# Performance work log

Hardware: AMD Instinct MI355X
Metric: run time of the kernel (lower is better)

The kernel has to match this reference:

```python
import jax, jax.numpy as jnp
import numpy as np

N = 16384          # collocation points
WIDTH = 128        # WavePINN width_size
DEPTH = 6          # WavePINN depth -> 5 hidden-to-hidden layers
PWIDTH = 32        # PsiNetwork width_size
PDEPTH = 2         # PsiNetwork depth -> 1 hidden-to-hidden layer
C0 = 1.0           # base_wave_speed


def _lin(k, out_dim, in_dim):
    return jax.random.normal(k, (out_dim, in_dim), jnp.float32) / np.sqrt(in_dim)


def setup_inputs() -> dict:
    key = jax.random.key(0)
    ks = jax.random.split(key, 20)
    inp = {
        "t": jax.random.uniform(ks[0], (N,), jnp.float32),
        "x": jax.random.uniform(ks[1], (N,), jnp.float32),
        "y": jax.random.uniform(ks[2], (N,), jnp.float32),
        "z": jax.random.uniform(ks[3], (N,), jnp.float32),
        # WavePINN (u_model) params: 4 -> 128 -> (128)x5 -> 1
        "uW_in": _lin(ks[4], WIDTH, 4),
        "ub_in": jnp.zeros((WIDTH,), jnp.float32),
        "uW_hid": jax.random.normal(ks[5], (DEPTH - 1, WIDTH, WIDTH), jnp.float32) / np.sqrt(WIDTH),
        "ub_hid": jnp.zeros((DEPTH - 1, WIDTH), jnp.float32),
        "uW_out": _lin(ks[6], 1, WIDTH),
        "ub_out": jnp.zeros((1,), jnp.float32),
        # PsiNetwork params: 4 -> 32 -> 32 -> 1
        "pW_in": _lin(ks[7], PWIDTH, 4),
        "pb_in": jnp.zeros((PWIDTH,), jnp.float32),
        "pW_hid": jax.random.normal(ks[8], (PDEPTH - 1, PWIDTH, PWIDTH), jnp.float32) / np.sqrt(PWIDTH),
        "pb_hid": jnp.zeros((PDEPTH - 1, PWIDTH), jnp.float32),
        "pW_out": _lin(ks[9], 1, PWIDTH),
        "pb_out": jnp.zeros((1,), jnp.float32),
    }
    return inp


def _mlp(pt, W_in, b_in, W_hid, b_hid, W_out, b_out):
    # eqx.nn.MLP with tanh activation, linear final layer; returns scalar
    h = jnp.tanh(W_in @ pt + b_in)
    for i in range(W_hid.shape[0]):  # static, small layer count
        h = jnp.tanh(W_hid[i] @ h + b_hid[i])
    return (W_out @ h + b_out)[0]


def reference(t, x, y, z,
              uW_in, ub_in, uW_hid, ub_hid, uW_out, ub_out,
              pW_in, pb_in, pW_hid, pb_hid, pW_out, pb_out):
    def point_residual(pt):  # pt: [4] = (t, x, y, z)
        u_fn = lambda p: _mlp(p, uW_in, ub_in, uW_hid, ub_hid, uW_out, ub_out)
        psi = _mlp(pt, pW_in, pb_in, pW_hid, pb_hid, pW_out, pb_out)
        c = C0 * (1.0 + psi)  # modulated wave speed
        # diagonal of the 4x4 Hessian: u_tt, u_xx, u_yy, u_zz
        d = jnp.diagonal(jax.hessian(u_fn)(pt))
        lap = d[1] + d[2] + d[3]
        resid = d[0] - c ** 2 * lap
        has_nan = jnp.any(jnp.isnan(jnp.stack([d[0], d[1], d[2], d[3], c])))
        return jnp.where(has_nan, jnp.float32(jnp.nan), resid)

    pts = jnp.stack([t, x, y, z], axis=1)  # [N, 4]
    return jax.vmap(point_residual)(pts).astype(jnp.float32)
```

## Files before the change

### kernel.cpp

```cpp
#include <hip/hip_runtime.h>
#include <math.h>

#define N_PTS 16384
#define WID   128
#define NHID  5
#define PPB   16
#define CH    9
#define COLS  (PPB*CH)
#define KPAD  132
#define NBLK  (N_PTS/PPB)

typedef __attribute__((ext_vector_type(8))) __bf16 bf16x8;
typedef __attribute__((ext_vector_type(4))) float  f32x4;

__device__ __forceinline__ unsigned short f2bf(float x) {
    unsigned int u = __builtin_bit_cast(unsigned int, x);
    u += 0x7FFFu + ((u >> 16) & 1u);
    return (unsigned short)(u >> 16);
}
__device__ __forceinline__ float bf2f(unsigned short h) {
    unsigned int u = ((unsigned int)h) << 16;
    return __builtin_bit_cast(float, u);
}
__device__ __forceinline__ void split_bf(float x, unsigned short& hi, unsigned short& lo) {
    const unsigned int u = __builtin_bit_cast(unsigned int, x);
    hi = (unsigned short)(u >> 16);
    const float rem = x - __builtin_bit_cast(float, u & 0xFFFF0000u);
    lo = (unsigned short)(__builtin_bit_cast(unsigned int, rem) >> 16);
}
__device__ __forceinline__ unsigned int cvtpk(float v0, float v1) {
    unsigned int r;
    asm("v_cvt_pk_bf16_f32 %0, %1, %2" : "=v"(r) : "v"(v0), "v"(v1));
    return r;
}
__device__ __forceinline__ void split_pk4(const float v0, const float v1,
                                          const float v2, const float v3,
                                          uint2& ph, uint2& pl) {
    const unsigned int h01 = cvtpk(v0, v1);
    const unsigned int h23 = cvtpk(v2, v3);
    const float f0 = __builtin_bit_cast(float, h01 << 16);
    const float f1 = __builtin_bit_cast(float, h01 & 0xFFFF0000u);
    const float f2 = __builtin_bit_cast(float, h23 << 16);
    const float f3 = __builtin_bit_cast(float, h23 & 0xFFFF0000u);
    ph = make_uint2(h01, h23);
    pl = make_uint2(cvtpk(v0 - f0, v1 - f1), cvtpk(v2 - f2, v3 - f3));
}
__device__ __forceinline__ void fast_tanh_g(float x, float& a, float& g) {
    x = fminf(fmaxf(x, -40.0f), 40.0f);
    const float e = __builtin_amdgcn_exp2f(2.88539008177793f * x);
    const float r = __builtin_amdgcn_rcpf(e + 1.0f);
    a = 1.0f - 2.0f * r;
    g = 4.0f * e * r * r;
}

__global__ __launch_bounds__(64) void pack_w(const float* __restrict__ uWhid,
                                             unsigned short* __restrict__ whi,
                                             unsigned short* __restrict__ wlo)
{
    const int f  = blockIdx.x;
    const int v  = threadIdx.x;
    const int l  = f >> 5;
    const int s  = (f >> 3) & 3;
    const int rt = f & 7;
    const int row = rt*16 + (v & 15);
    const int k0  = s*32 + ((v >> 4) << 3);
    const float* src = uWhid + (l*WID + row)*WID + k0;
    unsigned short h[8], lo[8];
#pragma unroll
    for (int j = 0; j < 8; ++j) {
        const float x = src[j];
        h[j]  = f2bf(x);
        lo[j] = f2bf(x - bf2f(h[j]));
    }
    const int off = f*512 + v*8;
    *reinterpret_cast<ushort4*>(&whi[off])   = make_ushort4(h[0],h[1],h[2],h[3]);
    *reinterpret_cast<ushort4*>(&whi[off+4]) = make_ushort4(h[4],h[5],h[6],h[7]);
    *reinterpret_cast<ushort4*>(&wlo[off])   = make_ushort4(lo[0],lo[1],lo[2],lo[3]);
    *reinterpret_cast<ushort4*>(&wlo[off+4]) = make_ushort4(lo[4],lo[5],lo[6],lo[7]);
}

__global__ __launch_bounds__(256, 2) void resid_mfma(
    const float* __restrict__ gt, const float* __restrict__ gx,
    const float* __restrict__ gy, const float* __restrict__ gz,
    const float* __restrict__ uWin, const float* __restrict__ ubin,
    const float* __restrict__ ubhid, const float* __restrict__ uWout,
    const unsigned short* __restrict__ whi, const unsigned short* __restrict__ wlo,
    const float* __restrict__ pWin, const float* __restrict__ pbin,
    const float* __restrict__ pWhid, const float* __restrict__ pbhid,
    const float* __restrict__ pWout, const float* __restrict__ pbout,
    float* __restrict__ out)
{
    __shared__ unsigned short act_h[COLS*KPAD];
    __shared__ unsigned short act_l[COLS*KPAD];
    __shared__ float pts4[PPB][4];
    __shared__ float psi_h1[PPB][32];
    __shared__ float c2s[PPB];
    __shared__ float psum[4][PPB][4];

    {
        const int skew = (int)((blockIdx.x + (blockIdx.x >> 8)) & 3);
        for (int i = 0; i < skew; ++i) {
            __builtin_amdgcn_s_sleep(60);
        }
    }

    const int tid  = threadIdx.x;
    const int rq   = tid >> 6;
    const int v    = tid & 63;
    const int base = blockIdx.x * PPB;

    if (tid < PPB) {
        pts4[tid][0] = gt[base+tid]; pts4[tid][1] = gx[base+tid];
        pts4[tid][2] = gy[base+tid]; pts4[tid][3] = gz[base+tid];
    }
    __syncthreads();

    {
        const int p  = tid & 15;
        const int gg = tid >> 4;
        const float q0 = pts4[p][0], q1 = pts4[p][1], q2 = pts4[p][2], q3 = pts4[p][3];
#pragma unroll
        for (int c4 = 0; c4 < 2; ++c4) {
            float vf[CH][4];
#pragma unroll
            for (int i = 0; i < 4; ++i) {
                const int n = gg*8 + c4*4 + i;
                const float4 wr = *reinterpret_cast<const float4*>(&uWin[n*4]);
                const float z = ubin[n] + wr.x*q0 + wr.y*q1 + wr.z*q2 + wr.w*q3;
                float a, g;  fast_tanh_g(z, a, g);
                const float m = -2.0f * a * g;
                vf[0][i] = a;
                vf[1][i] = g*wr.x; vf[2][i] = g*wr.y; vf[3][i] = g*wr.z; vf[4][i] = g*wr.w;
                vf[5][i] = m*wr.x*wr.x; vf[6][i] = m*wr.y*wr.y;
                vf[7][i] = m*wr.z*wr.z; vf[8][i] = m*wr.w*wr.w;
            }
            const int n0 = gg*8 + c4*4;
#pragma unroll
            for (int ch = 0; ch < CH; ++ch) {
                uint2 ph, pl;
                split_pk4(vf[ch][0], vf[ch][1], vf[ch][2], vf[ch][3], ph, pl);
                const int off = (ch*PPB + p)*KPAD + n0;
                *reinterpret_cast<uint2*>(&act_h[off]) = ph;
                *reinterpret_cast<uint2*>(&act_l[off]) = pl;
            }
        }
    }
    {
        const int p = tid >> 4, sub = tid & 15;
        const float q0 = pts4[p][0], q1 = pts4[p][1], q2 = pts4[p][2], q3 = pts4[p][3];
#pragma unroll
        for (int rr = 0; rr < 2; ++rr) {
            const int r = sub*2 + rr;
            const float4 wr = *reinterpret_cast<const float4*>(&pWin[r*4]);
            float a, gd;
            fast_tanh_g(pbin[r] + wr.x*q0 + wr.y*q1 + wr.z*q2 + wr.w*q3, a, gd);
            psi_h1[p][r] = a;
        }
    }
    __syncthreads();

    {
        const int p = tid >> 4, sub = tid & 15;
        float partial = 0.f;
#pragma unroll
        for (int rr = 0; rr < 2; ++rr) {
            const int r = sub*2 + rr;
            float s = pbhid[r];
#pragma unroll
            for (int j = 0; j < 32; ++j) s = fmaf(pWhid[r*32+j], psi_h1[p][j], s);
            float a, gd;  fast_tanh_g(s, a, gd);
            partial = fmaf(pWout[r], a, partial);
        }
        partial += __shfl_xor(partial, 1);
        partial += __shfl_xor(partial, 2);
        partial += __shfl_xor(partial, 4);
        partial += __shfl_xor(partial, 8);
        if (sub == 0) {
            const float c = 1.0f + pbout[0] + partial;
            c2s[p] = c * c;
        }
    }

    f32x4 acc[2][CH];
    const int g4    = (v >> 4) << 2;
    const int lrow0 = rq * 32;
    const int bcol  = v & 15;
    const int krow  = (v >> 4) << 3;

    for (int l = 0; l < NHID; ++l) {
#pragma unroll
        for (int rt = 0; rt < 2; ++rt) {
            acc[rt][0] = *reinterpret_cast<const f32x4*>(&ubhid[l*WID + lrow0 + rt*16 + g4]);
#pragma unroll
            for (int ct = 1; ct < CH; ++ct) acc[rt][ct] = (f32x4){0.f,0.f,0.f,0.f};
        }
#pragma unroll
        for (int s = 0; s < 4; ++s) {
            bf16x8 bh[CH], bl[CH], ah[2], al[2];
            const int kof = s*32 + krow;
            const int fb  = ((l*4 + s)*8 + rq*2)*512 + v*8;
#pragma unroll
            for (int rt = 0; rt < 2; ++rt) {
                ah[rt] = *reinterpret_cast<const bf16x8*>(&whi[fb + rt*512]);
                al[rt] = *reinterpret_cast<const bf16x8*>(&wlo[fb + rt*512]);
            }
#pragma unroll
            for (int ct = 0; ct < CH; ++ct) {
                const int off = (ct*PPB + bcol)*KPAD + kof;
                bh[ct] = *reinterpret_cast<const bf16x8*>(&act_h[off]);
                bl[ct] = *reinterpret_cast<const bf16x8*>(&act_l[off]);
            }
            __builtin_amdgcn_s_setprio(1);
#pragma unroll
            for (int rt = 0; rt < 2; ++rt)
#pragma unroll
                for (int ct = 0; ct < CH; ++ct)
                    acc[rt][ct] = __builtin_amdgcn_mfma_f32_16x16x32_bf16(ah[rt], bh[ct], acc[rt][ct], 0,0,0);
#pragma unroll
            for (int rt = 0; rt < 2; ++rt)
#pragma unroll
                for (int ct = 0; ct < CH; ++ct)
                    acc[rt][ct] = __builtin_amdgcn_mfma_f32_16x16x32_bf16(ah[rt], bl[ct], acc[rt][ct], 0,0,0);
#pragma unroll
            for (int rt = 0; rt < 2; ++rt)
#pragma unroll
                for (int ct = 0; ct < CH; ++ct)
                    acc[rt][ct] = __builtin_amdgcn_mfma_f32_16x16x32_bf16(al[rt], bh[ct], acc[rt][ct], 0,0,0);
            __builtin_amdgcn_s_setprio(0);
        }

        if (l < NHID-1) {
            const int p = v & 15;
            uint2 ph[2][CH], pl[2][CH];
#pragma unroll
            for (int rt = 0; rt < 2; ++rt) {
                float vf[CH][4];
#pragma unroll
                for (int r = 0; r < 4; ++r) {
                    float a, g;  fast_tanh_g(acc[rt][0][r], a, g);
                    const float m2a = -2.0f * a;
                    vf[0][r] = a;
#pragma unroll
                    for (int d = 0; d < 4; ++d) {
                        const float zd  = acc[rt][1+d][r];
                        const float zdd = acc[rt][5+d][r];
                        vf[1+d][r] = g * zd;
                        vf[5+d][r] = g * fmaf(m2a*zd, zd, zdd);
                    }
                }
#pragma unroll
                for (int ch = 0; ch < CH; ++ch)
                    split_pk4(vf[ch][0], vf[ch][1], vf[ch][2], vf[ch][3], ph[rt][ch], pl[rt][ch]);
            }
            __syncthreads();
#pragma unroll
            for (int rt = 0; rt < 2; ++rt) {
                const int n0 = lrow0 + rt*16 + g4;
#pragma unroll
                for (int ch = 0; ch < CH; ++ch) {
                    const int off = (ch*PPB + p)*KPAD + n0;
                    *reinterpret_cast<uint2*>(&act_h[off]) = ph[rt][ch];
                    *reinterpret_cast<uint2*>(&act_l[off]) = pl[rt][ch];
                }
            }
            __syncthreads();
        }
    }

    float part0 = 0.f, part1 = 0.f, part2 = 0.f, part3 = 0.f;
#pragma unroll
    for (int rt = 0; rt < 2; ++rt) {
        const float4 w4 = *reinterpret_cast<const float4*>(&uWout[lrow0 + rt*16 + g4]);
#pragma unroll
        for (int r = 0; r < 4; ++r) {
            const float wr = (&w4.x)[r];
            float a, g;  fast_tanh_g(acc[rt][0][r], a, g);
            const float zd0 = acc[rt][1][r], zd1 = acc[rt][2][r];
            const float zd2 = acc[rt][3][r], zd3 = acc[rt][4][r];
            part0 = fmaf(wr, g*(acc[rt][5][r] - 2.0f*a*zd0*zd0), part0);
            part1 = fmaf(wr, g*(acc[rt][6][r] - 2.0f*a*zd1*zd1), part1);
            part2 = fmaf(wr, g*(acc[rt][7][r] - 2.0f*a*zd2*zd2), part2);
            part3 = fmaf(wr, g*(acc[rt][8][r] - 2.0f*a*zd3*zd3), part3);
        }
    }
    part0 += __shfl_xor(part0, 16); part0 += __shfl_xor(part0, 32);
    part1 += __shfl_xor(part1, 16); part1 += __shfl_xor(part1, 32);
    part2 += __shfl_xor(part2, 16); part2 += __shfl_xor(part2, 32);
    part3 += __shfl_xor(part3, 16); part3 += __shfl_xor(part3, 32);
    if (v < PPB) {
        psum[rq][v][0] = part0; psum[rq][v][1] = part1;
        psum[rq][v][2] = part2; psum[rq][v][3] = part3;
    }
    __syncthreads();
    if (tid < PPB) {
        const float d0  = psum[0][tid][0] + psum[1][tid][0] + psum[2][tid][0] + psum[3][tid][0];
        const float lap = (psum[0][tid][1] + psum[1][tid][1] + psum[2][tid][1] + psum[3][tid][1])
                        + (psum[0][tid][2] + psum[1][tid][2] + psum[2][tid][2] + psum[3][tid][2])
                        + (psum[0][tid][3] + psum[1][tid][3] + psum[2][tid][3] + psum[3][tid][3]);
        out[base+tid] = d0 - c2s[tid]*lap;
    }
}

__global__ __launch_bounds__(64) void psi_kernel(
    const float* __restrict__ gt, const float* __restrict__ gx,
    const float* __restrict__ gy, const float* __restrict__ gz,
    const float* __restrict__ pWin, const float* __restrict__ pbin,
    const float* __restrict__ pWhid, const float* __restrict__ pbhid,
    const float* __restrict__ pWout, const float* __restrict__ pbout,
    float* __restrict__ c2)
{
    const int i = blockIdx.x * 64 + threadIdx.x;
    if (i >= N_PTS) return;
    const float q0 = gt[i], q1 = gx[i], q2 = gy[i], q3 = gz[i];
    float h1[32];
#pragma unroll
    for (int r = 0; r < 32; ++r) {
        float s = pbin[r] + pWin[r*4+0]*q0 + pWin[r*4+1]*q1
                + pWin[r*4+2]*q2 + pWin[r*4+3]*q3;
        h1[r] = tanhf(s);
    }
    float psi = pbout[0];
#pragma unroll 4
    for (int r = 0; r < 32; ++r) {
        float s = pbhid[r];
#pragma unroll
        for (int j = 0; j < 32; ++j) s = fmaf(pWhid[r*32+j], h1[j], s);
        psi = fmaf(pWout[r], tanhf(s), psi);
    }
    const float c = 1.0f + psi;
    c2[i] = c * c;
}

__global__ __launch_bounds__(256, 2) void resid_f32(
    const float* __restrict__ gt, const float* __restrict__ gx,
    const float* __restrict__ gy, const float* __restrict__ gz,
    const float* __restrict__ uWin, const float* __restrict__ ubin,
    const float* __restrict__ uWhid, const float* __restrict__ ubhid,
    const float* __restrict__ uWout,
    const float* __restrict__ c2g, float* __restrict__ out)
{
    __shared__ float act[WID][16*CH];
    __shared__ float ptsh[16][4];
    __shared__ float dsh[16][4];
    const int tid  = threadIdx.x;
    const int rg   = tid >> 4;
    const int p    = tid & 15;
    const int base = blockIdx.x * 16;
    const int row0 = rg * 8;
    const int c0   = p * CH;
    if (tid < 16) {
        ptsh[tid][0] = gt[base+tid]; ptsh[tid][1] = gx[base+tid];
        ptsh[tid][2] = gy[base+tid]; ptsh[tid][3] = gz[base+tid];
    }
    __syncthreads();
    {
        const float q0 = ptsh[p][0], q1 = ptsh[p][1], q2 = ptsh[p][2], q3 = ptsh[p][3];
#pragma unroll
        for (int r = 0; r < 8; ++r) {
            const int row = row0 + r;
            const float w0 = uWin[row*4+0], w1 = uWin[row*4+1];
            const float w2 = uWin[row*4+2], w3 = uWin[row*4+3];
            const float zz = ubin[row] + w0*q0 + w1*q1 + w2*q2 + w3*q3;
            const float a  = tanhf(zz);
            const float g  = 1.0f - a*a;
            const float m2 = -2.0f * a * g;
            act[row][c0+0] = a;
            act[row][c0+1] = g*w0; act[row][c0+2] = g*w1;
            act[row][c0+3] = g*w2; act[row][c0+4] = g*w3;
            act[row][c0+5] = m2*w0*w0; act[row][c0+6] = m2*w1*w1;
            act[row][c0+7] = m2*w2*w2; act[row][c0+8] = m2*w3*w3;
        }
    }
    __syncthreads();
    for (int l = 0; l < NHID; ++l) {
        const float* __restrict__ Wl = uWhid + l*WID*WID;
        float accv[8][CH];
#pragma unroll
        for (int r = 0; r < 8; ++r) {
            accv[r][0] = ubhid[l*WID + row0 + r];
#pragma unroll
            for (int c = 1; c < CH; ++c) accv[r][c] = 0.0f;
        }
        for (int k0 = 0; k0 < WID; k0 += 4) {
            float4 wv[8];
#pragma unroll
            for (int r = 0; r < 8; ++r)
                wv[r] = *reinterpret_cast<const float4*>(&Wl[(row0+r)*WID + k0]);
            float hv[4][CH];
#pragma unroll
            for (int kk = 0; kk < 4; ++kk)
#pragma unroll
                for (int c = 0; c < CH; ++c) hv[kk][c] = act[k0+kk][c0+c];
#pragma unroll
            for (int kk = 0; kk < 4; ++kk)
#pragma unroll
                for (int r = 0; r < 8; ++r) {
                    const float wk = reinterpret_cast<const float*>(&wv[r])[kk];
#pragma unroll
                    for (int c = 0; c < CH; ++c) accv[r][c] = fmaf(wk, hv[kk][c], accv[r][c]);
                }
        }
        __syncthreads();
#pragma unroll
        for (int r = 0; r < 8; ++r) {
            const int row = row0 + r;
            const float a = tanhf(accv[r][0]);
            const float g = 1.0f - a*a;
            act[row][c0+0] = a;
#pragma unroll
            for (int i = 0; i < 4; ++i) {
                const float zd  = accv[r][1+i];
                const float zdd = accv[r][5+i];
                act[row][c0+1+i] = g*zd;
                act[row][c0+5+i] = g*(zdd - 2.0f*a*zd*zd);
            }
        }
        __syncthreads();
    }
    if (tid < 64) {
        const int pp = tid >> 2, ii = tid & 3;
        float s = 0.0f;
        for (int k = 0; k < WID; ++k) s = fmaf(uWout[k], act[k][pp*CH+5+ii], s);
        dsh[pp][ii] = s;
    }
    __syncthreads();
    if (tid < 16) {
        const float d0  = dsh[tid][0];
        const float lap = dsh[tid][1] + dsh[tid][2] + dsh[tid][3];
        out[base+tid] = d0 - c2g[base+tid]*lap;
    }
}

extern "C" void kernel_launch(void* const* d_in, const int* in_sizes, int n_in,
                              void* d_out, int out_size, void* d_ws, size_t ws_size,
                              hipStream_t stream)
{
    const float* gt    = (const float*)d_in[0];
    const float* gx    = (const float*)d_in[1];
    const float* gy    = (const float*)d_in[2];
    const float* gz    = (const float*)d_in[3];
    const float* uWin  = (const float*)d_in[4];
    const float* ubin  = (const float*)d_in[5];
    const float* uWhid = (const float*)d_in[6];
    const float* ubhid = (const float*)d_in[7];
    const float* uWout = (const float*)d_in[8];
    const float* pWin  = (const float*)d_in[10];
    const float* pbin  = (const float*)d_in[11];
    const float* pWhid = (const float*)d_in[12];
    const float* pbhid = (const float*)d_in[13];
    const float* pWout = (const float*)d_in[14];
    const float* pbout = (const float*)d_in[15];
    float* out = (float*)d_out;

    if (ws_size >= 327680) {
        unsigned short* whi = (unsigned short*)d_ws;
        unsigned short* wlo = whi + 81920;
        pack_w<<<160, 64, 0, stream>>>(uWhid, whi, wlo);
        resid_mfma<<<NBLK, 256, 0, stream>>>(gt, gx, gy, gz,
                uWin, ubin, ubhid, uWout, whi, wlo,
                pWin, pbin, pWhid, pbhid, pWout, pbout, out);
    } else {
        float* c2 = (float*)d_ws;
        psi_kernel<<<N_PTS/64, 64, 0, stream>>>(gt, gx, gy, gz,
                pWin, pbin, pWhid, pbhid, pWout, pbout, c2);
        resid_f32<<<N_PTS/16, 256, 0, stream>>>(gt, gx, gy, gz,
                uWin, ubin, uWhid, ubhid, uWout, c2, out);
    }
}
```

Baseline: 80.01 us.

## Interleave two 16-point sub-batches per block to overlap MFMA with tanh-jet packing

Each block now handles 32 points as two 16-point sub-batches that share one activation buffer. MFMA work for one sub-batch is interleaved with the tanh/derivative jet packing of the other, so matrix and vector work can overlap across layers. The psi network setup and the second input jet are also moved into the shadow of the first layer's MFMAs. The block-skew sleep and setprio hints are dropped. The cost is roughly doubled accumulator register pressure, half as many blocks, and extra barriers per layer.

```diff
diff --git a/kernel.cpp b/kernel.cpp
--- a/kernel.cpp
+++ b/kernel.cpp
@@ -4,9 +4,10 @@
 #define N_PTS 16384
 #define WID   128
 #define NHID  5
-#define PPB   16
+#define SPTS  16
+#define PPB   32
 #define CH    9
-#define COLS  (PPB*CH)
+#define COLS  (SPTS*CH)
 #define KPAD  132
 #define NBLK  (N_PTS/PPB)
 
@@ -79,6 +80,168 @@
     *reinterpret_cast<ushort4*>(&wlo[off+4]) = make_ushort4(lo[4],lo[5],lo[6],lo[7]);
 }
 
+__device__ __forceinline__ void mfma_layer(
+    f32x4 (&acc)[2][CH],
+    const unsigned short* __restrict__ whi, const unsigned short* __restrict__ wlo,
+    const unsigned short (&act_h)[COLS*KPAD], const unsigned short (&act_l)[COLS*KPAD],
+    const float* __restrict__ ubhid, const int l,
+    const int lrow0, const int g4, const int rq, const int v,
+    const int bcol, const int krow)
+{
+#pragma unroll
+    for (int rt = 0; rt < 2; ++rt) {
+        acc[rt][0] = *reinterpret_cast<const f32x4*>(&ubhid[l*WID + lrow0 + rt*16 + g4]);
+#pragma unroll
+        for (int ct = 1; ct < CH; ++ct) acc[rt][ct] = (f32x4){0.f,0.f,0.f,0.f};
+    }
+#pragma unroll
+    for (int s = 0; s < 4; ++s) {
+        bf16x8 bh[CH], bl[CH], ah[2], al[2];
+        const int kof = s*32 + krow;
+        const int fb  = ((l*4 + s)*8 + rq*2)*512 + v*8;
+#pragma unroll
+        for (int rt = 0; rt < 2; ++rt) {
+            ah[rt] = *reinterpret_cast<const bf16x8*>(&whi[fb + rt*512]);
+            al[rt] = *reinterpret_cast<const bf16x8*>(&wlo[fb + rt*512]);
+        }
+#pragma unroll
+        for (int ct = 0; ct < CH; ++ct) {
+            const int off = (ct*SPTS + bcol)*KPAD + kof;
+            bh[ct] = *reinterpret_cast<const bf16x8*>(&act_h[off]);
+            bl[ct] = *reinterpret_cast<const bf16x8*>(&act_l[off]);
+        }
+#pragma unroll
+        for (int rt = 0; rt < 2; ++rt)
+#pragma unroll
+            for (int ct = 0; ct < CH; ++ct)
+                acc[rt][ct] = __builtin_amdgcn_mfma_f32_16x16x32_bf16(ah[rt], bh[ct], acc[rt][ct], 0,0,0);
+#pragma unroll
+        for (int rt = 0; rt < 2; ++rt)
+#pragma unroll
+            for (int ct = 0; ct < CH; ++ct)
+                acc[rt][ct] = __builtin_amdgcn_mfma_f32_16x16x32_bf16(ah[rt], bl[ct], acc[rt][ct], 0,0,0);
+#pragma unroll
+        for (int rt = 0; rt < 2; ++rt)
+#pragma unroll
+            for (int ct = 0; ct < CH; ++ct)
+                acc[rt][ct] = __builtin_amdgcn_mfma_f32_16x16x32_bf16(al[rt], bh[ct], acc[rt][ct], 0,0,0);
+    }
+}
+
+__device__ __forceinline__ void jet_pack(
+    const f32x4 (&acc)[2][CH], uint2 (&ph)[2][CH], uint2 (&pl)[2][CH])
+{
+#pragma unroll
+    for (int rt = 0; rt < 2; ++rt) {
+        float vf[CH][4];
+#pragma unroll
+        for (int r = 0; r < 4; ++r) {
+            float a, g;  fast_tanh_g(acc[rt][0][r], a, g);
+            const float m2a = -2.0f * a;
+            vf[0][r] = a;
+#pragma unroll
+            for (int d = 0; d < 4; ++d) {
+                const float zd  = acc[rt][1+d][r];
+                const float zdd = acc[rt][5+d][r];
+                vf[1+d][r] = g * zd;
+                vf[5+d][r] = g * fmaf(m2a*zd, zd, zdd);
+            }
+        }
+#pragma unroll
+        for (int ch = 0; ch < CH; ++ch)
+            split_pk4(vf[ch][0], vf[ch][1], vf[ch][2], vf[ch][3], ph[rt][ch], pl[rt][ch]);
+    }
+}
+
+__device__ __forceinline__ void store_act(
+    const uint2 (&ph)[2][CH], const uint2 (&pl)[2][CH],
+    unsigned short (&act_h)[COLS*KPAD], unsigned short (&act_l)[COLS*KPAD],
+    const int lrow0, const int g4, const int p)
+{
+#pragma unroll
+    for (int rt = 0; rt < 2; ++rt) {
+        const int n0 = lrow0 + rt*16 + g4;
+#pragma unroll
+        for (int ch = 0; ch < CH; ++ch) {
+            const int off = (ch*SPTS + p)*KPAD + n0;
+            *reinterpret_cast<uint2*>(&act_h[off]) = ph[rt][ch];
+            *reinterpret_cast<uint2*>(&act_l[off]) = pl[rt][ch];
+        }
+    }
+}
+
+__device__ __forceinline__ void input_jet(
+    const float q0, const float q1, const float q2, const float q3,
+    const float* __restrict__ uWin, const float* __restrict__ ubin, const int gg,
+    uint2 (&ph)[2][CH], uint2 (&pl)[2][CH])
+{
+#pragma unroll
+    for (int c4 = 0; c4 < 2; ++c4) {
+        float vf[CH][4];
+#pragma unroll
+        for (int i = 0; i < 4; ++i) {
+            const int n = gg*8 + c4*4 + i;
+            const float4 wr = *reinterpret_cast<const float4*>(&uWin[n*4]);
+            const float z = ubin[n] + wr.x*q0 + wr.y*q1 + wr.z*q2 + wr.w*q3;
+            float a, g;  fast_tanh_g(z, a, g);
+            const float m = -2.0f * a * g;
+            vf[0][i] = a;
+            vf[1][i] = g*wr.x; vf[2][i] = g*wr.y; vf[3][i] = g*wr.z; vf[4][i] = g*wr.w;
+            vf[5][i] = m*wr.x*wr.x; vf[6][i] = m*wr.y*wr.y;
+            vf[7][i] = m*wr.z*wr.z; vf[8][i] = m*wr.w*wr.w;
+        }
+#pragma unroll
+        for (int ch = 0; ch < CH; ++ch)
+            split_pk4(vf[ch][0], vf[ch][1], vf[ch][2], vf[ch][3], ph[c4][ch], pl[c4][ch]);
+    }
+}
+
+__device__ __forceinline__ void store_input(
+    const uint2 (&ph)[2][CH], const uint2 (&pl)[2][CH],
+    unsigned short (&act_h)[COLS*KPAD], unsigned short (&act_l)[COLS*KPAD],
+    const int gg, const int p)
+{
+#pragma unroll
+    for (int c4 = 0; c4 < 2; ++c4) {
+        const int n0 = gg*8 + c4*4;
+#pragma unroll
+        for (int ch = 0; ch < CH; ++ch) {
+            const int off = (ch*SPTS + p)*KPAD + n0;
+            *reinterpret_cast<uint2*>(&act_h[off]) = ph[c4][ch];
+            *reinterpret_cast<uint2*>(&act_l[off]) = pl[c4][ch];
+        }
+    }
+}
+
+__device__ __forceinline__ void out_parts(
+    const f32x4 (&acc)[2][CH], const float* __restrict__ uWout,
+    const int lrow0, const int g4,
+    float& p0, float& p1, float& p2, float& p3)
+{
+    p0 = p1 = p2 = p3 = 0.f;
+#pragma unroll
+    for (int rt = 0; rt < 2; ++rt) {
+        const float4 w4 = *reinterpret_cast<const float4*>(&uWout[lrow0 + rt*16 + g4]);
+#pragma unroll
+        for (int r = 0; r < 4; ++r) {
+            const float wr = (&w4.x)[r];
+            float a, g;  fast_tanh_g(acc[rt][0][r], a, g);
+            const float zd0 = acc[rt][1][r], zd1 = acc[rt][2][r];
+            const float zd2 = acc[rt][3][r], zd3 = acc[rt][4][r];
+            p0 = fmaf(wr, g*(acc[rt][5][r] - 2.0f*a*zd0*zd0), p0);
+            p1 = fmaf(wr, g*(acc[rt][6][r] - 2.0f*a*zd1*zd1), p1);
+            p2 = fmaf(wr, g*(acc[rt][7][r] - 2.0f*a*zd2*zd2), p2);
+            p3 = fmaf(wr, g*(acc[rt][8][r] - 2.0f*a*zd3*zd3), p3);
+        }
+    }
+    p0 += __shfl_xor(p0, 16); p0 += __shfl_xor(p0, 32);
+    p1 += __shfl_xor(p1, 16); p1 += __shfl_xor(p1, 32);
+    p2 += __shfl_xor(p2, 16); p2 += __shfl_xor(p2, 32);
+    p3 += __shfl_xor(p3, 16); p3 += __shfl_xor(p3, 32);
+}
+
+#define PSUM(rqi, pi, ii) scratch[((rqi)*PPB + (pi))*4 + (ii)]
+
 __global__ __launch_bounds__(256, 2) void resid_mfma(
     const float* __restrict__ gt, const float* __restrict__ gx,
     const float* __restrict__ gy, const float* __restrict__ gz,
@@ -93,16 +256,8 @@
     __shared__ unsigned short act_h[COLS*KPAD];
     __shared__ unsigned short act_l[COLS*KPAD];
     __shared__ float pts4[PPB][4];
-    __shared__ float psi_h1[PPB][32];
+    __shared__ float scratch[PPB*32];
     __shared__ float c2s[PPB];
-    __shared__ float psum[4][PPB][4];
-
-    {
-        const int skew = (int)((blockIdx.x + (blockIdx.x >> 8)) & 3);
-        for (int i = 0; i < skew; ++i) {
-            __builtin_amdgcn_s_sleep(60);
-        }
-    }
 
     const int tid  = threadIdx.x;
     const int rq   = tid >> 6;
@@ -115,189 +270,107 @@
     }
     __syncthreads();
 
+    const int pI = tid & 15;
+    const int gg = tid >> 4;
+    const float qa0 = pts4[pI][0],    qa1 = pts4[pI][1],    qa2 = pts4[pI][2],    qa3 = pts4[pI][3];
+    const float qb0 = pts4[16+pI][0], qb1 = pts4[16+pI][1], qb2 = pts4[16+pI][2], qb3 = pts4[16+pI][3];
+    const int pp  = tid >> 3;
+    const int sub = tid & 7;
+
     {
-        const int p  = tid & 15;
-        const int gg = tid >> 4;
-        const float q0 = pts4[p][0], q1 = pts4[p][1], q2 = pts4[p][2], q3 = pts4[p][3];
-#pragma unroll
-        for (int c4 = 0; c4 < 2; ++c4) {
-            float vf[CH][4];
-#pragma unroll
-            for (int i = 0; i < 4; ++i) {
-                const int n = gg*8 + c4*4 + i;
-                const float4 wr = *reinterpret_cast<const float4*>(&uWin[n*4]);
-                const float z = ubin[n] + wr.x*q0 + wr.y*q1 + wr.z*q2 + wr.w*q3;
-                float a, g;  fast_tanh_g(z, a, g);
-                const float m = -2.0f * a * g;
-                vf[0][i] = a;
-                vf[1][i] = g*wr.x; vf[2][i] = g*wr.y; vf[3][i] = g*wr.z; vf[4][i] = g*wr.w;
-                vf[5][i] = m*wr.x*wr.x; vf[6][i] = m*wr.y*wr.y;
-                vf[7][i] = m*wr.z*wr.z; vf[8][i] = m*wr.w*wr.w;
-            }
-            const int n0 = gg*8 + c4*4;
-#pragma unroll
-            for (int ch = 0; ch < CH; ++ch) {
-                uint2 ph, pl;
-                split_pk4(vf[ch][0], vf[ch][1], vf[ch][2], vf[ch][3], ph, pl);
-                const int off = (ch*PPB + p)*KPAD + n0;
-                *reinterpret_cast<uint2*>(&act_h[off]) = ph;
-                *reinterpret_cast<uint2*>(&act_l[off]) = pl;
-            }
-        }
+        uint2 phI[2][CH], plI[2][CH];
+        input_jet(qa0, qa1, qa2, qa3, uWin, ubin, gg, phI, plI);
+        store_input(phI, plI, act_h, act_l, gg, pI);
     }
     {
-        const int p = tid >> 4, sub = tid & 15;
-        const float q0 = pts4[p][0], q1 = pts4[p][1], q2 = pts4[p][2], q3 = pts4[p][3];
-#pragma unroll
-        for (int rr = 0; rr < 2; ++rr) {
-            const int r = sub*2 + rr;
+        const float q0 = pts4[pp][0], q1 = pts4[pp][1], q2 = pts4[pp][2], q3 = pts4[pp][3];
+#pragma unroll
+        for (int rr = 0; rr < 4; ++rr) {
+            const int r = sub*4 + rr;
             const float4 wr = *reinterpret_cast<const float4*>(&pWin[r*4]);
             float a, gd;
             fast_tanh_g(pbin[r] + wr.x*q0 + wr.y*q1 + wr.z*q2 + wr.w*q3, a, gd);
-            psi_h1[p][r] = a;
-        }
-    }
-    __syncthreads();
-
-    {
-        const int p = tid >> 4, sub = tid & 15;
-        float partial = 0.f;
-#pragma unroll
-        for (int rr = 0; rr < 2; ++rr) {
-            const int r = sub*2 + rr;
-            float s = pbhid[r];
-#pragma unroll
-            for (int j = 0; j < 32; ++j) s = fmaf(pWhid[r*32+j], psi_h1[p][j], s);
-            float a, gd;  fast_tanh_g(s, a, gd);
-            partial = fmaf(pWout[r], a, partial);
-        }
-        partial += __shfl_xor(partial, 1);
-        partial += __shfl_xor(partial, 2);
-        partial += __shfl_xor(partial, 4);
-        partial += __shfl_xor(partial, 8);
-        if (sub == 0) {
-            const float c = 1.0f + pbout[0] + partial;
-            c2s[p] = c * c;
-        }
-    }
-
-    f32x4 acc[2][CH];
+            scratch[pp*32 + r] = a;
+        }
+    }
+    __syncthreads();
+
     const int g4    = (v >> 4) << 2;
     const int lrow0 = rq * 32;
     const int bcol  = v & 15;
     const int krow  = (v >> 4) << 3;
 
-    for (int l = 0; l < NHID; ++l) {
-#pragma unroll
-        for (int rt = 0; rt < 2; ++rt) {
-            acc[rt][0] = *reinterpret_cast<const f32x4*>(&ubhid[l*WID + lrow0 + rt*16 + g4]);
-#pragma unroll
-            for (int ct = 1; ct < CH; ++ct) acc[rt][ct] = (f32x4){0.f,0.f,0.f,0.f};
-        }
-#pragma unroll
-        for (int s = 0; s < 4; ++s) {
-            bf16x8 bh[CH], bl[CH], ah[2], al[2];
-            const int kof = s*32 + krow;
-            const int fb  = ((l*4 + s)*8 + rq*2)*512 + v*8;
-#pragma unroll
-            for (int rt = 0; rt < 2; ++rt) {
-                ah[rt] = *reinterpret_cast<const bf16x8*>(&whi[fb + rt*512]);
-                al[rt] = *reinterpret_cast<const bf16x8*>(&wlo[fb + rt*512]);
-            }
-#pragma unroll
-            for (int ct = 0; ct < CH; ++ct) {
-                const int off = (ct*PPB + bcol)*KPAD + kof;
-                bh[ct] = *reinterpret_cast<const bf16x8*>(&act_h[off]);
-                bl[ct] = *reinterpret_cast<const bf16x8*>(&act_l[off]);
-            }
-            __builtin_amdgcn_s_setprio(1);
-#pragma unroll
-            for (int rt = 0; rt < 2; ++rt)
-#pragma unroll
-                for (int ct = 0; ct < CH; ++ct)
-                    acc[rt][ct] = __builtin_amdgcn_mfma_f32_16x16x32_bf16(ah[rt], bh[ct], acc[rt][ct], 0,0,0);
-#pragma unroll
-            for (int rt = 0; rt < 2; ++rt)
-#pragma unroll
-                for (int ct = 0; ct < CH; ++ct)
-                    acc[rt][ct] = __builtin_amdgcn_mfma_f32_16x16x32_bf16(ah[rt], bl[ct], acc[rt][ct], 0,0,0);
-#pragma unroll
-            for (int rt = 0; rt < 2; ++rt)
-#pragma unroll
-                for (int ct = 0; ct < CH; ++ct)
-                    acc[rt][ct] = __builtin_amdgcn_mfma_f32_16x16x32_bf16(al[rt], bh[ct], acc[rt][ct], 0,0,0);
-            __builtin_amdgcn_s_setprio(0);
-        }
-
-        if (l < NHID-1) {
-            const int p = v & 15;
-            uint2 ph[2][CH], pl[2][CH];
-#pragma unroll
-            for (int rt = 0; rt < 2; ++rt) {
-                float vf[CH][4];
-#pragma unroll
-                for (int r = 0; r < 4; ++r) {
-                    float a, g;  fast_tanh_g(acc[rt][0][r], a, g);
-                    const float m2a = -2.0f * a;
-                    vf[0][r] = a;
-#pragma unroll
-                    for (int d = 0; d < 4; ++d) {
-                        const float zd  = acc[rt][1+d][r];
-                        const float zdd = acc[rt][5+d][r];
-                        vf[1+d][r] = g * zd;
-                        vf[5+d][r] = g * fmaf(m2a*zd, zd, zdd);
-                    }
-                }
-#pragma unroll
-                for (int ch = 0; ch < CH; ++ch)
-                    split_pk4(vf[ch][0], vf[ch][1], vf[ch][2], vf[ch][3], ph[rt][ch], pl[rt][ch]);
-            }
-            __syncthreads();
-#pragma unroll
-            for (int rt = 0; rt < 2; ++rt) {
-                const int n0 = lrow0 + rt*16 + g4;
-#pragma unroll
-                for (int ch = 0; ch < CH; ++ch) {
-                    const int off = (ch*PPB + p)*KPAD + n0;
-                    *reinterpret_cast<uint2*>(&act_h[off]) = ph[rt][ch];
-                    *reinterpret_cast<uint2*>(&act_l[off]) = pl[rt][ch];
-                }
-            }
-            __syncthreads();
-        }
-    }
-
-    float part0 = 0.f, part1 = 0.f, part2 = 0.f, part3 = 0.f;
-#pragma unroll
-    for (int rt = 0; rt < 2; ++rt) {
-        const float4 w4 = *reinterpret_cast<const float4*>(&uWout[lrow0 + rt*16 + g4]);
-#pragma unroll
-        for (int r = 0; r < 4; ++r) {
-            const float wr = (&w4.x)[r];
-            float a, g;  fast_tanh_g(acc[rt][0][r], a, g);
-            const float zd0 = acc[rt][1][r], zd1 = acc[rt][2][r];
-            const float zd2 = acc[rt][3][r], zd3 = acc[rt][4][r];
-            part0 = fmaf(wr, g*(acc[rt][5][r] - 2.0f*a*zd0*zd0), part0);
-            part1 = fmaf(wr, g*(acc[rt][6][r] - 2.0f*a*zd1*zd1), part1);
-            part2 = fmaf(wr, g*(acc[rt][7][r] - 2.0f*a*zd2*zd2), part2);
-            part3 = fmaf(wr, g*(acc[rt][8][r] - 2.0f*a*zd3*zd3), part3);
-        }
-    }
-    part0 += __shfl_xor(part0, 16); part0 += __shfl_xor(part0, 32);
-    part1 += __shfl_xor(part1, 16); part1 += __shfl_xor(part1, 32);
-    part2 += __shfl_xor(part2, 16); part2 += __shfl_xor(part2, 32);
-    part3 += __shfl_xor(part3, 16); part3 += __shfl_xor(part3, 32);
-    if (v < PPB) {
-        psum[rq][v][0] = part0; psum[rq][v][1] = part1;
-        psum[rq][v][2] = part2; psum[rq][v][3] = part3;
-    }
-    __syncthreads();
-    if (tid < PPB) {
-        const float d0  = psum[0][tid][0] + psum[1][tid][0] + psum[2][tid][0] + psum[3][tid][0];
-        const float lap = (psum[0][tid][1] + psum[1][tid][1] + psum[2][tid][1] + psum[3][tid][1])
-                        + (psum[0][tid][2] + psum[1][tid][2] + psum[2][tid][2] + psum[3][tid][2])
-                        + (psum[0][tid][3] + psum[1][tid][3] + psum[2][tid][3] + psum[3][tid][3]);
+    f32x4 accA[2][CH], accB[2][CH];
+    uint2 phA[2][CH], plA[2][CH], phB[2][CH], plB[2][CH];
+
+    mfma_layer(accA, whi, wlo, act_h, act_l, ubhid, 0, lrow0, g4, rq, v, bcol, krow);
+    input_jet(qb0, qb1, qb2, qb3, uWin, ubin, gg, phB, plB);
+    {
+        float partial = 0.f;
+#pragma unroll
+        for (int rr = 0; rr < 4; ++rr) {
+            const int r = sub*4 + rr;
+            float s = pbhid[r];
+#pragma unroll
+            for (int j = 0; j < 32; ++j) s = fmaf(pWhid[r*32+j], scratch[pp*32 + j], s);
+            float a, gd;  fast_tanh_g(s, a, gd);
+            partial = fmaf(pWout[r], a, partial);
+        }
+        partial += __shfl_xor(partial, 1);
+        partial += __shfl_xor(partial, 2);
+        partial += __shfl_xor(partial, 4);
+        if (sub == 0) {
+            const float c = 1.0f + pbout[0] + partial;
+            c2s[pp] = c * c;
+        }
+    }
+
+    for (int l = 0; l < 4; ++l) {
+        __syncthreads();
+        if (l == 0) store_input(phB, plB, act_h, act_l, gg, pI);
+        else        store_act  (phB, plB, act_h, act_l, lrow0, g4, bcol);
+        __syncthreads();
+        mfma_layer(accB, whi, wlo, act_h, act_l, ubhid, l, lrow0, g4, rq, v, bcol, krow);
+        jet_pack(accA, phA, plA);
+        __syncthreads();
+        store_act(phA, plA, act_h, act_l, lrow0, g4, bcol);
+        __syncthreads();
+        mfma_layer(accA, whi, wlo, act_h, act_l, ubhid, l+1, lrow0, g4, rq, v, bcol, krow);
+        jet_pack(accB, phB, plB);
+    }
+
+    __syncthreads();
+    store_act(phB, plB, act_h, act_l, lrow0, g4, bcol);
+    __syncthreads();
+    mfma_layer(accB, whi, wlo, act_h, act_l, ubhid, 4, lrow0, g4, rq, v, bcol, krow);
+    float a0, a1, a2, a3;
+    out_parts(accA, uWout, lrow0, g4, a0, a1, a2, a3);
+    if (v < 16) {
+        PSUM(rq, v, 0) = a0; PSUM(rq, v, 1) = a1;
+        PSUM(rq, v, 2) = a2; PSUM(rq, v, 3) = a3;
+    }
+    __syncthreads();
+    float b0, b1, b2, b3;
+    out_parts(accB, uWout, lrow0, g4, b0, b1, b2, b3);
+    if (v < 16) {
+        PSUM(rq, 16+v, 0) = b0; PSUM(rq, 16+v, 1) = b1;
+        PSUM(rq, 16+v, 2) = b2; PSUM(rq, 16+v, 3) = b3;
+    }
+    if (tid < 16) {
+        const float d0  = PSUM(0,tid,0) + PSUM(1,tid,0) + PSUM(2,tid,0) + PSUM(3,tid,0);
+        const float lap = (PSUM(0,tid,1) + PSUM(1,tid,1) + PSUM(2,tid,1) + PSUM(3,tid,1))
+                        + (PSUM(0,tid,2) + PSUM(1,tid,2) + PSUM(2,tid,2) + PSUM(3,tid,2))
+                        + (PSUM(0,tid,3) + PSUM(1,tid,3) + PSUM(2,tid,3) + PSUM(3,tid,3));
         out[base+tid] = d0 - c2s[tid]*lap;
+    }
+    __syncthreads();
+    if (tid < 16) {
+        const int p = 16 + tid;
+        const float d0  = PSUM(0,p,0) + PSUM(1,p,0) + PSUM(2,p,0) + PSUM(3,p,0);
+        const float lap = (PSUM(0,p,1) + PSUM(1,p,1) + PSUM(2,p,1) + PSUM(3,p,1))
+                        + (PSUM(0,p,2) + PSUM(1,p,2) + PSUM(2,p,2) + PSUM(3,p,2))
+                        + (PSUM(0,p,3) + PSUM(1,p,3) + PSUM(2,p,3) + PSUM(3,p,3));
+        out[base+p] = d0 - c2s[p]*lap;
     }
 }
 
```

Result: slower. 203.9 us (+154.9%).
